# Kernel optimization log

Measured on AMD Instinct MI355X. Metric: run time of the kernel, lower is better.

The kernel has to match this reference:

```python
import jax, jax.numpy as jnp
from jax import lax
import numpy as np

NS, NC = 12, 4            # n_state, n_ctrl
NSC = NS + NC             # tau = [x; u]
T, B = 50, 2048
U_LO, U_HI = -1.0, 1.0
LQR_ITERS = 3             # qp_iter-style outer LQR iterations
N_LS = 5                  # max_linesearch_iter
LS_DECAY = 0.5            # linesearch_decay


def setup_inputs() -> dict:
    key = jax.random.key(0)
    k0, k1, k2, k3, k4 = jax.random.split(key, 5)
    x0 = jax.random.normal(k0, (B, NS), jnp.float32)
    # PD quadratic cost: C = 0.1 * A A^T + I  (symmetric positive definite)
    A = jax.random.normal(k1, (T, B, NSC, NSC), jnp.float32) * (1.0 / np.sqrt(NSC))
    C = 0.1 * jnp.einsum('tbik,tbjk->tbij', A, A) + jnp.eye(NSC, dtype=jnp.float32)
    c = jax.random.normal(k2, (T, B, NSC), jnp.float32)
    # Near-identity stable linear dynamics x' = F [x;u] + f
    F = 0.02 * jax.random.normal(k3, (T, B, NS, NSC), jnp.float32)
    eye_pad = jnp.concatenate([0.98 * jnp.eye(NS, dtype=jnp.float32),
                               jnp.zeros((NS, NC), jnp.float32)], axis=-1)
    F = F + eye_pad
    f = 0.01 * jax.random.normal(k4, (T, B, NS), jnp.float32)
    return {'x0': x0, 'C': C, 'c': c, 'F': F, 'f': f}


def _riccati(C, c, F, f):
    """Backward Riccati recursion. Returns feedback gains K [T,B,NC,NS], k [T,B,NC]."""
    def step(carry, inp):
        V, v = carry                      # V: [B,NS,NS], v: [B,NS]
        Ct, ct, Ft, ft = inp
        FtV = jnp.einsum('bki,bkl->bil', Ft, V)          # F^T V: [B,NSC,NS]
        Q = Ct + jnp.einsum('bil,blj->bij', FtV, Ft)     # [B,NSC,NSC]
        q = ct + jnp.einsum('bki,bk->bi', Ft,
                            jnp.einsum('bij,bj->bi', V, ft) + v)
        Qxx, Qxu = Q[:, :NS, :NS], Q[:, :NS, NS:]
        Qux, Quu = Q[:, NS:, :NS], Q[:, NS:, NS:]
        qx, qu = q[:, :NS], q[:, NS:]
        rhs = jnp.concatenate([Qux, qu[:, :, None]], axis=-1)  # [B,NC,NS+1]
        sol = jnp.linalg.solve(Quu, rhs)
        K = -sol[:, :, :NS]               # [B,NC,NS]
        kk = -sol[:, :, NS]               # [B,NC]
        QxuK = jnp.einsum('bij,bjk->bik', Qxu, K)
        V_new = Qxx + QxuK + QxuK.transpose(0, 2, 1) \
            + jnp.einsum('bji,bjl,blk->bik', K, Quu, K)
        V_new = 0.5 * (V_new + V_new.transpose(0, 2, 1))
        v_new = qx + jnp.einsum('bij,bj->bi', Qxu, kk) \
            + jnp.einsum('bji,bj->bi', K, qu + jnp.einsum('bij,bj->bi', Quu, kk))
        return (V_new, v_new), (K, kk)

    Vz = jnp.zeros((C.shape[1], NS, NS), C.dtype)
    vz = jnp.zeros((C.shape[1], NS), C.dtype)
    _, (K, kk) = lax.scan(step, (Vz, vz), (C, c, F, f), reverse=True)
    return K, kk


def _rollout(alpha, x0, u_nom, K, kk, C, c, F, f):
    """Forward pass with box-clamped controls and line-search blending."""
    def step(carry, inp):
        x, cost = carry
        Ct, ct, Ft, ft, Kt, kt, unomt = inp
        u_lqr = jnp.einsum('bij,bj->bi', Kt, x) + kt
        u = jnp.clip((1.0 - alpha) * unomt + alpha * u_lqr, U_LO, U_HI)
        tau = jnp.concatenate([x, u], axis=-1)            # [B,NSC]
        cost = cost + 0.5 * jnp.einsum('bi,bij,bj->b', tau, Ct, tau) \
            + jnp.einsum('bi,bi->b', ct, tau)
        x_next = jnp.einsum('bij,bj->bi', Ft, tau) + ft
        return (x_next, cost), tau

    init = (x0, jnp.zeros(x0.shape[0], x0.dtype))
    (_, cost), taus = lax.scan(step, init, (C, c, F, f, K, kk, u_nom))
    return cost, taus  # cost [B], taus [T,B,NSC]


def reference(x0, C, c, F, f):
    alphas = LS_DECAY ** jnp.arange(N_LS, dtype=C.dtype)  # [N_LS]
    u_nom = jnp.zeros((T, x0.shape[0], NC), x0.dtype)
    taus = None
    for _ in range(LQR_ITERS):
        K, kk = _riccati(C, c, F, f)
        costs, taus_all = jax.vmap(
            lambda a: _rollout(a, x0, u_nom, K, kk, C, c, F, f))(alphas)
        # costs: [N_LS,B]; taus_all: [N_LS,T,B,NSC]. Pick best alpha per batch elem.
        best = jnp.argmin(costs, axis=0)                  # [B]
        taus = jnp.take_along_axis(taus_all,
                                   best[None, None, :, None], axis=0)[0]
        u_nom = taus[:, :, NS:]
    return taus  # [T, B, NSC] optimized trajectory [x; u]
```

## Files before the change

kernel.cpp:

```cpp
#include <hip/hip_runtime.h>
#include <math.h>

#define T_   50
#define B_   2048
#define NS_  12
#define NC_  4
#define NSC_ 16
#define LDC  20
#define AST  808

__device__ __forceinline__ float dot4f(const float4 a, const float4 b) {
    return a.x*b.x + a.y*b.y + a.z*b.z + a.w*b.w;
}
__device__ __forceinline__ void axpy4(float4& acc, float s, const float4 v) {
    acc.x += s*v.x; acc.y += s*v.y; acc.z += s*v.z; acc.w += s*v.w;
}

__device__ __forceinline__ void wsync() {
    __builtin_amdgcn_wave_barrier();
    __builtin_amdgcn_s_waitcnt(0xC07F);
    __builtin_amdgcn_wave_barrier();
}

struct RicPref { float4 rC, rAux; };

__device__ __forceinline__ RicPref ric_load(
    const float* Cg, const float* cg, const float* Fg, const float* fg,
    int t, int b, int lane)
{
    RicPref p;
    const size_t base = (size_t)t * B_ + b;
    p.rC = ((const float4*)(Cg + base*256))[lane];
    if (lane < 48)      p.rAux = ((const float4*)(Fg + base*192))[lane];
    else if (lane < 52) p.rAux = ((const float4*)(cg + base*16))[lane-48];
    else if (lane < 55) p.rAux = ((const float4*)(fg + base*12))[lane-52];
    return p;
}

__global__ __launch_bounds__(64) void riccati_kernel(
    const float* __restrict__ Cg, const float* __restrict__ cg,
    const float* __restrict__ Fg, const float* __restrict__ fg,
    float* __restrict__ Kk)
{
    const int b    = blockIdx.x;
    const int lane = threadIdx.x;

    __shared__ __align__(16) float sV[144];
    __shared__ __align__(16) float sv[12];
    __shared__ __align__(16) float sF[12*LDC];
    __shared__ __align__(16) float sc[16];
    __shared__ __align__(16) float sf[12];
    __shared__ __align__(16) float sP[12*LDC];
    __shared__ __align__(16) float sQ[16*LDC];
    __shared__ __align__(16) float sq[16];
    __shared__ __align__(16) float stmp[12];
    __shared__ __align__(16) float sK[48];
    __shared__ __align__(16) float skk[4];
    __shared__ __align__(16) float sM[144];

    for (int i = lane; i < 144; i += 64) sV[i] = 0.f;
    if (lane < 12) sv[lane] = 0.f;

    RicPref cur = ric_load(Cg, cg, Fg, fg, T_-1, b, lane);
    wsync();

    for (int t = T_ - 1; t >= 0; --t) {
        const size_t base = (size_t)t * B_ + b;

        wsync();
        const float4 rCq = cur.rC;
        {
            const int row = lane >> 2, ch = (lane & 3) << 2;
            if (lane < 48)      *(float4*)(sF + row*LDC + ch) = cur.rAux;
            else if (lane < 52) ((float4*)sc)[lane-48] = cur.rAux;
            else if (lane < 55) ((float4*)sf)[lane-52] = cur.rAux;
        }
        RicPref nxt = ric_load(Cg, cg, Fg, fg, (t > 0) ? t-1 : 0, b, lane);
        wsync();

        if (lane < 48) {
            const int k = lane >> 2, jc = (lane & 3) << 2;
            const float4 v0 = *(const float4*)(sV + k*12);
            const float4 v1 = *(const float4*)(sV + k*12 + 4);
            const float4 v2 = *(const float4*)(sV + k*12 + 8);
            const float vk[12] = {v0.x,v0.y,v0.z,v0.w, v1.x,v1.y,v1.z,v1.w,
                                  v2.x,v2.y,v2.z,v2.w};
            float4 acc = make_float4(0.f,0.f,0.f,0.f);
            #pragma unroll
            for (int l = 0; l < 12; ++l) {
                axpy4(acc, vk[l], *(const float4*)(sF + l*LDC + jc));
            }
            *(float4*)(sP + k*LDC + jc) = acc;
            if (jc == 0) {
                float accT = sv[k];
                #pragma unroll
                for (int l = 0; l < 12; ++l) accT += vk[l] * sf[l];
                stmp[k] = accT;
            }
        }
        wsync();

        {
            const int i = lane >> 2, jc = (lane & 3) << 2;
            float4 acc = rCq;
            float fcol[12];
            #pragma unroll
            for (int k = 0; k < 12; ++k) {
                fcol[k] = sF[k*LDC + i];
                axpy4(acc, fcol[k], *(const float4*)(sP + k*LDC + jc));
            }
            *(float4*)(sQ + i*LDC + jc) = acc;
            if (jc == 0) {
                float accq = sc[i];
                #pragma unroll
                for (int k = 0; k < 12; ++k) accq += fcol[k] * stmp[k];
                sq[i] = accq;
            }
        }
        wsync();

        {
            const float* Qu = sQ + 12*LDC + 12;
            const float a00=Qu[0],      a01=Qu[1],      a02=Qu[2],      a03=Qu[3];
            const float a11=Qu[LDC+1],  a12=Qu[LDC+2],  a13=Qu[LDC+3];
            const float a22=Qu[2*LDC+2],a23=Qu[2*LDC+3],a33=Qu[3*LDC+3];
            const float l00 = sqrtf(a00), i00 = 1.f/l00;
            const float l10 = a01*i00, l20 = a02*i00, l30 = a03*i00;
            const float l11 = sqrtf(a11 - l10*l10), i11 = 1.f/l11;
            const float l21 = (a12 - l20*l10)*i11;
            const float l31 = (a13 - l30*l10)*i11;
            const float l22 = sqrtf(a22 - l20*l20 - l21*l21), i22 = 1.f/l22;
            const float l32 = (a23 - l30*l20 - l31*l21)*i22;
            const float l33 = sqrtf(a33 - l30*l30 - l31*l31 - l32*l32), i33 = 1.f/l33;
            if (lane < 13) {
                float r0, r1, r2, r3;
                if (lane < 12) {
                    r0 = sQ[12*LDC + lane]; r1 = sQ[13*LDC + lane];
                    r2 = sQ[14*LDC + lane]; r3 = sQ[15*LDC + lane];
                } else {
                    r0 = sq[12]; r1 = sq[13]; r2 = sq[14]; r3 = sq[15];
                }
                const float y0 = r0*i00;
                const float y1 = (r1 - l10*y0)*i11;
                const float y2 = (r2 - l20*y0 - l21*y1)*i22;
                const float y3 = (r3 - l30*y0 - l31*y1 - l32*y2)*i33;
                const float z3 = y3*i33;
                const float z2 = (y2 - l32*z3)*i22;
                const float z1 = (y1 - l21*z2 - l31*z3)*i11;
                const float z0 = (y0 - l10*z1 - l20*z2 - l30*z3)*i00;
                if (lane < 12) {
                    sK[0*12+lane] = -z0; sK[1*12+lane] = -z1;
                    sK[2*12+lane] = -z2; sK[3*12+lane] = -z3;
                } else {
                    skk[0] = -z0; skk[1] = -z1; skk[2] = -z2; skk[3] = -z3;
                }
            }
        }
        wsync();

        if (lane < 52) {
            (Kk + base*52)[lane] = (lane < 48) ? sK[lane] : skk[lane-48];
        }
        if (lane < 36) {
            const int i = lane / 3, jc = (lane % 3) << 2;
            float4 acc = make_float4(0.f,0.f,0.f,0.f);
            #pragma unroll
            for (int m = 0; m < 4; ++m) {
                axpy4(acc, sK[m*12 + i], *(const float4*)(sQ + (12+m)*LDC + jc));
            }
            *(float4*)(sM + i*12 + jc) = acc;
        } else if (lane < 48) {
            const int i = lane - 36;
            float acc = sq[i];
            #pragma unroll
            for (int m = 0; m < 4; ++m) acc += sQ[i*LDC + 12 + m] * skk[m];
            sv[i] = acc;
        }
        wsync();

        if (lane < 36) {
            const int i = lane / 3, jc = (lane % 3) << 2;
            const float4 q  = *(const float4*)(sQ + i*LDC + jc);
            const float4 m1 = *(const float4*)(sM + i*12 + jc);
            const float t0 = sM[(jc+0)*12 + i];
            const float t1 = sM[(jc+1)*12 + i];
            const float t2 = sM[(jc+2)*12 + i];
            const float t3 = sM[(jc+3)*12 + i];
            float4 r;
            r.x = q.x + 0.5f*(m1.x + t0);
            r.y = q.y + 0.5f*(m1.y + t1);
            r.z = q.z + 0.5f*(m1.z + t2);
            r.w = q.w + 0.5f*(m1.w + t3);
            *(float4*)(sV + i*12 + jc) = r;
        }
        cur = nxt;
    }
}

struct Pref {
    float4 C0, C1, C2, C3;
    float4 D0, D1, D2, D3;
    float4 F0, F1, F2, F3;
    float4 K0, K1, K2;
    float  kk, ci, c2i, fi;
};

__device__ __forceinline__ Pref pload(
    const float* Cg, const float* cg, const float* Fg, const float* fg,
    const float* Kk, int t, int b, int i, bool ul)
{
    Pref p;
    const size_t base = (size_t)t * B_ + b;
    const float4* Cr = (const float4*)(Cg + base*256 + i*16);
    p.C0 = Cr[0]; p.C1 = Cr[1]; p.C2 = Cr[2]; p.C3 = Cr[3];
    const float4* Fr = (const float4*)(Fg + base*192 + i*16);
    p.F0 = Fr[0]; p.F1 = Fr[1]; p.F2 = Fr[2]; p.F3 = Fr[3];
    p.ci = cg[base*16 + i];
    p.fi = fg[base*12 + i];
    if (ul) {
        const float4* Dr = (const float4*)(Cg + base*256 + (12+i)*16);
        p.D0 = Dr[0]; p.D1 = Dr[1]; p.D2 = Dr[2]; p.D3 = Dr[3];
        const float4* Kr = (const float4*)(Kk + base*52 + i*12);
        p.K0 = Kr[0]; p.K1 = Kr[1]; p.K2 = Kr[2];
        p.kk  = Kk[base*52 + 48 + i];
        p.c2i = cg[base*16 + 12 + i];
    }
    return p;
}

__global__ __launch_bounds__(64) void rollout_kernel(
    const float* __restrict__ x0g, const float* __restrict__ Cg,
    const float* __restrict__ cg,  const float* __restrict__ Fg,
    const float* __restrict__ fg,  const float* __restrict__ Kk,
    float* __restrict__ outg)
{
    const int b    = blockIdx.x;
    const int lane = threadIdx.x;
    int a = lane / 12;
    int i = lane - a*12;
    const bool act = (lane < 60);
    if (!act) { a = 4; i = lane - 52; }
    const bool ulane = act && (i < 4);
    const float alpha = ldexpf(1.0f, -a);

    __shared__ __align__(16) float staus[5*AST];
    __shared__ __align__(16) float sunom[T_*NC_];
    __shared__ __align__(16) float spart[64];
    __shared__ __align__(16) float scost[8];
    __shared__ int sbest;

    const float x0v = x0g[b*12 + i];
    if (lane < 50) *(float4*)(sunom + lane*4) = make_float4(0.f,0.f,0.f,0.f);

    Pref cur = pload(Cg, cg, Fg, fg, Kk, 0, b, i, ulane);
    wsync();

    for (int iter = 0; iter < 3; ++iter) {
        float xv   = x0v;
        float cacc = 0.f;

        for (int t = 0; t < T_; ++t) {
            float* tb = staus + a*AST + t*16;
            if (act) tb[i] = xv;
            Pref nxt = pload(Cg, cg, Fg, fg, Kk, (t+1 < T_) ? t+1 : 0, b, i, ulane);
            wsync();
            const float4 xA = *(const float4*)(tb);
            const float4 xB = *(const float4*)(tb + 4);
            const float4 xC = *(const float4*)(tb + 8);
            if (ulane) {
                const float ulqr = dot4f(cur.K0, xA) + dot4f(cur.K1, xB)
                                 + dot4f(cur.K2, xC) + cur.kk;
                const float un = sunom[t*4 + i];
                float u = (1.f - alpha)*un + alpha*ulqr;
                u = fminf(1.f, fmaxf(-1.f, u));
                tb[12 + i] = u;
            }
            wsync();
            const float4 uA = *(const float4*)(tb + 12);
            const float cc = dot4f(cur.C0, xA) + dot4f(cur.C1, xB)
                           + dot4f(cur.C2, xC) + dot4f(cur.C3, uA);
            cacc += (0.5f*cc + cur.ci) * xv;
            if (ulane) {
                const float cc2 = dot4f(cur.D0, xA) + dot4f(cur.D1, xB)
                                + dot4f(cur.D2, xC) + dot4f(cur.D3, uA);
                const float uval = (i == 0) ? uA.x : (i == 1) ? uA.y
                                 : (i == 2) ? uA.z : uA.w;
                cacc += (0.5f*cc2 + cur.c2i) * uval;
            }
            xv = dot4f(cur.F0, xA) + dot4f(cur.F1, xB)
               + dot4f(cur.F2, xC) + dot4f(cur.F3, uA) + cur.fi;
            cur = nxt;
        }

        spart[lane] = act ? cacc : 0.f;
        wsync();
        if (lane < 5) {
            float s = 0.f;
            #pragma unroll
            for (int j = 0; j < 12; ++j) s += spart[lane*12 + j];
            scost[lane] = s;
        }
        wsync();
        if (lane == 0) {
            int bi = 0; float bc = scost[0];
            #pragma unroll
            for (int aa = 1; aa < 5; ++aa) {
                if (scost[aa] < bc) { bc = scost[aa]; bi = aa; }
            }
            sbest = bi;
        }
        wsync();
        const int best = sbest;

        if (lane < 50) {
            const float4 uu = *(const float4*)(staus + best*AST + lane*16 + 12);
            *(float4*)(sunom + lane*4) = uu;
        }
        if (iter == 2 && lane < 50) {
            const float* src = staus + best*AST + lane*16;
            float* dst = outg + ((size_t)lane*B_ + b)*16;
            *(float4*)(dst)      = *(const float4*)(src);
            *(float4*)(dst + 4)  = *(const float4*)(src + 4);
            *(float4*)(dst + 8)  = *(const float4*)(src + 8);
            *(float4*)(dst + 12) = *(const float4*)(src + 12);
        }
        wsync();
    }
}

extern "C" void kernel_launch(void* const* d_in, const int* in_sizes, int n_in,
                              void* d_out, int out_size, void* d_ws, size_t ws_size,
                              hipStream_t stream) {
    const float* x0 = (const float*)d_in[0];
    const float* C  = (const float*)d_in[1];
    const float* c  = (const float*)d_in[2];
    const float* F  = (const float*)d_in[3];
    const float* f  = (const float*)d_in[4];
    float* out = (float*)d_out;
    float* Kk  = (float*)d_ws;

    riccati_kernel<<<B_, 64, 0, stream>>>(C, c, F, f, Kk);
    rollout_kernel<<<B_, 64, 0, stream>>>(x0, C, c, F, f, Kk, out);
}
```

Before: 477.5 us.

## Restructure rollout lane mapping with DPP reductions and transpose F in Riccati

The rollout kernel now assigns lanes by (row, 4-column chunk) and processes all five line-search alphas per lane. Matrix-vector products are reduced with DPP quad sums, and the cost argmin uses wave shuffles instead of shared-memory partials and extra barriers. Per-lane register prefetch drops from full C/D/F rows to one float4 each, aiming to cut register pressure and redundant loads. The Riccati kernel stores a transposed copy of F and keeps K transposed so column reads become vectorized float4 loads. This adds shared-memory writes and more complex indexing, and the new lane mapping risks subtle correctness errors.

```diff
diff --git a/kernel.cpp b/kernel.cpp
--- a/kernel.cpp
+++ b/kernel.cpp
@@ -20,6 +20,14 @@
     __builtin_amdgcn_wave_barrier();
     __builtin_amdgcn_s_waitcnt(0xC07F);
     __builtin_amdgcn_wave_barrier();
+}
+
+__device__ __forceinline__ float qsum(float v) {
+    v += __int_as_float(__builtin_amdgcn_update_dpp(
+            0, __float_as_int(v), 0xB1, 0xF, 0xF, true));
+    v += __int_as_float(__builtin_amdgcn_update_dpp(
+            0, __float_as_int(v), 0x4E, 0xF, 0xF, true));
+    return v;
 }
 
 struct RicPref { float4 rC, rAux; };
@@ -48,14 +56,14 @@
     __shared__ __align__(16) float sV[144];
     __shared__ __align__(16) float sv[12];
     __shared__ __align__(16) float sF[12*LDC];
+    __shared__ __align__(16) float sFT[16*12];
     __shared__ __align__(16) float sc[16];
     __shared__ __align__(16) float sf[12];
     __shared__ __align__(16) float sP[12*LDC];
     __shared__ __align__(16) float sQ[16*LDC];
     __shared__ __align__(16) float sq[16];
     __shared__ __align__(16) float stmp[12];
-    __shared__ __align__(16) float sK[48];
-    __shared__ __align__(16) float skk[4];
+    __shared__ __align__(16) float sKT[56];
     __shared__ __align__(16) float sM[144];
 
     for (int i = lane; i < 144; i += 64) sV[i] = 0.f;
@@ -70,8 +78,14 @@
         wsync();
         const float4 rCq = cur.rC;
         {
-            const int row = lane >> 2, ch = (lane & 3) << 2;
-            if (lane < 48)      *(float4*)(sF + row*LDC + ch) = cur.rAux;
+            const int row = lane >> 2, chx = lane & 3;
+            if (lane < 48) {
+                *(float4*)(sF + row*LDC + (chx<<2)) = cur.rAux;
+                sFT[(4*chx+0)*12 + row] = cur.rAux.x;
+                sFT[(4*chx+1)*12 + row] = cur.rAux.y;
+                sFT[(4*chx+2)*12 + row] = cur.rAux.z;
+                sFT[(4*chx+3)*12 + row] = cur.rAux.w;
+            }
             else if (lane < 52) ((float4*)sc)[lane-48] = cur.rAux;
             else if (lane < 55) ((float4*)sf)[lane-52] = cur.rAux;
         }
@@ -87,14 +101,14 @@
                                   v2.x,v2.y,v2.z,v2.w};
             float4 acc = make_float4(0.f,0.f,0.f,0.f);
             #pragma unroll
-            for (int l = 0; l < 12; ++l) {
+            for (int l = 0; l < 12; ++l)
                 axpy4(acc, vk[l], *(const float4*)(sF + l*LDC + jc));
-            }
             *(float4*)(sP + k*LDC + jc) = acc;
             if (jc == 0) {
-                float accT = sv[k];
-                #pragma unroll
-                for (int l = 0; l < 12; ++l) accT += vk[l] * sf[l];
+                float accT = sv[k]
+                    + dot4f(v0, *(const float4*)(sf))
+                    + dot4f(v1, *(const float4*)(sf+4))
+                    + dot4f(v2, *(const float4*)(sf+8));
                 stmp[k] = accT;
             }
         }
@@ -102,44 +116,46 @@
 
         {
             const int i = lane >> 2, jc = (lane & 3) << 2;
+            const float4 f0 = *(const float4*)(sFT + i*12);
+            const float4 f1 = *(const float4*)(sFT + i*12 + 4);
+            const float4 f2 = *(const float4*)(sFT + i*12 + 8);
+            const float fcol[12] = {f0.x,f0.y,f0.z,f0.w, f1.x,f1.y,f1.z,f1.w,
+                                    f2.x,f2.y,f2.z,f2.w};
             float4 acc = rCq;
-            float fcol[12];
             #pragma unroll
-            for (int k = 0; k < 12; ++k) {
-                fcol[k] = sF[k*LDC + i];
+            for (int k = 0; k < 12; ++k)
                 axpy4(acc, fcol[k], *(const float4*)(sP + k*LDC + jc));
-            }
             *(float4*)(sQ + i*LDC + jc) = acc;
             if (jc == 0) {
-                float accq = sc[i];
-                #pragma unroll
-                for (int k = 0; k < 12; ++k) accq += fcol[k] * stmp[k];
+                const float accq = sc[i]
+                    + dot4f(f0, *(const float4*)(stmp))
+                    + dot4f(f1, *(const float4*)(stmp+4))
+                    + dot4f(f2, *(const float4*)(stmp+8));
                 sq[i] = accq;
+                if (i >= 12) sQ[i*LDC + 16] = accq;
             }
         }
         wsync();
 
         {
-            const float* Qu = sQ + 12*LDC + 12;
-            const float a00=Qu[0],      a01=Qu[1],      a02=Qu[2],      a03=Qu[3];
-            const float a11=Qu[LDC+1],  a12=Qu[LDC+2],  a13=Qu[LDC+3];
-            const float a22=Qu[2*LDC+2],a23=Qu[2*LDC+3],a33=Qu[3*LDC+3];
-            const float l00 = sqrtf(a00), i00 = 1.f/l00;
-            const float l10 = a01*i00, l20 = a02*i00, l30 = a03*i00;
-            const float l11 = sqrtf(a11 - l10*l10), i11 = 1.f/l11;
-            const float l21 = (a12 - l20*l10)*i11;
-            const float l31 = (a13 - l30*l10)*i11;
-            const float l22 = sqrtf(a22 - l20*l20 - l21*l21), i22 = 1.f/l22;
-            const float l32 = (a23 - l30*l20 - l31*l21)*i22;
-            const float l33 = sqrtf(a33 - l30*l30 - l31*l31 - l32*l32), i33 = 1.f/l33;
+            const float4 u0 = *(const float4*)(sQ + 12*LDC + 12);
+            const float4 u1 = *(const float4*)(sQ + 13*LDC + 12);
+            const float4 u2 = *(const float4*)(sQ + 14*LDC + 12);
+            const float4 u3 = *(const float4*)(sQ + 15*LDC + 12);
+            const float l00 = sqrtf(u0.x), i00 = 1.f/l00;
+            const float l10 = u0.y*i00, l20 = u0.z*i00, l30 = u0.w*i00;
+            const float l11 = sqrtf(u1.y - l10*l10), i11 = 1.f/l11;
+            const float l21 = (u1.z - l20*l10)*i11;
+            const float l31 = (u1.w - l30*l10)*i11;
+            const float l22 = sqrtf(u2.z - l20*l20 - l21*l21), i22 = 1.f/l22;
+            const float l32 = (u2.w - l30*l20 - l31*l21)*i22;
+            const float l33 = sqrtf(u3.w - l30*l30 - l31*l31 - l32*l32), i33 = 1.f/l33;
             if (lane < 13) {
-                float r0, r1, r2, r3;
-                if (lane < 12) {
-                    r0 = sQ[12*LDC + lane]; r1 = sQ[13*LDC + lane];
-                    r2 = sQ[14*LDC + lane]; r3 = sQ[15*LDC + lane];
-                } else {
-                    r0 = sq[12]; r1 = sq[13]; r2 = sq[14]; r3 = sq[15];
-                }
+                const int cidx = (lane < 12) ? lane : 16;
+                const float r0 = sQ[12*LDC + cidx];
+                const float r1 = sQ[13*LDC + cidx];
+                const float r2 = sQ[14*LDC + cidx];
+                const float r3 = sQ[15*LDC + cidx];
                 const float y0 = r0*i00;
                 const float y1 = (r1 - l10*y0)*i11;
                 const float y2 = (r2 - l20*y0 - l21*y1)*i22;
@@ -148,33 +164,33 @@
                 const float z2 = (y2 - l32*z3)*i22;
                 const float z1 = (y1 - l21*z2 - l31*z3)*i11;
                 const float z0 = (y0 - l10*z1 - l20*z2 - l30*z3)*i00;
-                if (lane < 12) {
-                    sK[0*12+lane] = -z0; sK[1*12+lane] = -z1;
-                    sK[2*12+lane] = -z2; sK[3*12+lane] = -z3;
-                } else {
-                    skk[0] = -z0; skk[1] = -z1; skk[2] = -z2; skk[3] = -z3;
-                }
+                *(float4*)(sKT + lane*4) = make_float4(-z0,-z1,-z2,-z3);
             }
         }
         wsync();
 
         if (lane < 52) {
-            (Kk + base*52)[lane] = (lane < 48) ? sK[lane] : skk[lane-48];
+            float val;
+            if (lane < 48) {
+                const int i2 = lane / 12, j2 = lane - i2*12;
+                val = sKT[j2*4 + i2];
+            } else val = sKT[lane];
+            (Kk + base*52)[lane] = val;
         }
         if (lane < 36) {
             const int i = lane / 3, jc = (lane % 3) << 2;
+            const float4 kv = *(const float4*)(sKT + i*4);
             float4 acc = make_float4(0.f,0.f,0.f,0.f);
-            #pragma unroll
-            for (int m = 0; m < 4; ++m) {
-                axpy4(acc, sK[m*12 + i], *(const float4*)(sQ + (12+m)*LDC + jc));
-            }
+            axpy4(acc, kv.x, *(const float4*)(sQ + 12*LDC + jc));
+            axpy4(acc, kv.y, *(const float4*)(sQ + 13*LDC + jc));
+            axpy4(acc, kv.z, *(const float4*)(sQ + 14*LDC + jc));
+            axpy4(acc, kv.w, *(const float4*)(sQ + 15*LDC + jc));
             *(float4*)(sM + i*12 + jc) = acc;
         } else if (lane < 48) {
             const int i = lane - 36;
-            float acc = sq[i];
-            #pragma unroll
-            for (int m = 0; m < 4; ++m) acc += sQ[i*LDC + 12 + m] * skk[m];
-            sv[i] = acc;
+            const float4 qxu = *(const float4*)(sQ + i*LDC + 12);
+            const float4 kk4 = *(const float4*)(sKT + 48);
+            sv[i] = sq[i] + dot4f(qxu, kk4);
         }
         wsync();
 
@@ -186,44 +202,38 @@
             const float t1 = sM[(jc+1)*12 + i];
             const float t2 = sM[(jc+2)*12 + i];
             const float t3 = sM[(jc+3)*12 + i];
-            float4 r;
-            r.x = q.x + 0.5f*(m1.x + t0);
-            r.y = q.y + 0.5f*(m1.y + t1);
-            r.z = q.z + 0.5f*(m1.z + t2);
-            r.w = q.w + 0.5f*(m1.w + t3);
-            *(float4*)(sV + i*12 + jc) = r;
+            float4 rr;
+            rr.x = q.x + 0.5f*(m1.x + t0);
+            rr.y = q.y + 0.5f*(m1.y + t1);
+            rr.z = q.z + 0.5f*(m1.z + t2);
+            rr.w = q.w + 0.5f*(m1.w + t3);
+            *(float4*)(sV + i*12 + jc) = rr;
         }
         cur = nxt;
     }
 }
 
-struct Pref {
-    float4 C0, C1, C2, C3;
-    float4 D0, D1, D2, D3;
-    float4 F0, F1, F2, F3;
-    float4 K0, K1, K2;
-    float  kk, ci, c2i, fi;
-};
-
-__device__ __forceinline__ Pref pload(
-    const float* Cg, const float* cg, const float* Fg, const float* fg,
-    const float* Kk, int t, int b, int i, bool ul)
+struct RP { float4 C, F, K0, K1, K2; float kk, cr, fr; };
+
+__device__ __forceinline__ RP rp_load(
+    const float* __restrict__ Cg, const float* __restrict__ cg,
+    const float* __restrict__ Fg, const float* __restrict__ fg,
+    const float* __restrict__ Kg, int t, int b, int lane, int r)
 {
-    Pref p;
+    RP p;
     const size_t base = (size_t)t * B_ + b;
-    const float4* Cr = (const float4*)(Cg + base*256 + i*16);
-    p.C0 = Cr[0]; p.C1 = Cr[1]; p.C2 = Cr[2]; p.C3 = Cr[3];
-    const float4* Fr = (const float4*)(Fg + base*192 + i*16);
-    p.F0 = Fr[0]; p.F1 = Fr[1]; p.F2 = Fr[2]; p.F3 = Fr[3];
-    p.ci = cg[base*16 + i];
-    p.fi = fg[base*12 + i];
-    if (ul) {
-        const float4* Dr = (const float4*)(Cg + base*256 + (12+i)*16);
-        p.D0 = Dr[0]; p.D1 = Dr[1]; p.D2 = Dr[2]; p.D3 = Dr[3];
-        const float4* Kr = (const float4*)(Kk + base*52 + i*12);
-        p.K0 = Kr[0]; p.K1 = Kr[1]; p.K2 = Kr[2];
-        p.kk  = Kk[base*52 + 48 + i];
-        p.c2i = cg[base*16 + 12 + i];
+    p.C  = ((const float4*)(Cg + base*256))[lane];
+    p.cr = cg[base*16 + r];
+    if (lane < 48) {
+        p.F  = ((const float4*)(Fg + base*192))[lane];
+        p.fr = fg[base*12 + r];
+    }
+    if (lane < 20) {
+        const float* Kr = Kg + base*52 + (lane & 3)*12;
+        p.K0 = *(const float4*)(Kr);
+        p.K1 = *(const float4*)(Kr + 4);
+        p.K2 = *(const float4*)(Kr + 8);
+        p.kk = Kg[base*52 + 48 + (lane & 3)];
     }
     return p;
 }
@@ -236,86 +246,78 @@
 {
     const int b    = blockIdx.x;
     const int lane = threadIdx.x;
-    int a = lane / 12;
-    int i = lane - a*12;
-    const bool act = (lane < 60);
-    if (!act) { a = 4; i = lane - 52; }
-    const bool ulane = act && (i < 4);
-    const float alpha = ldexpf(1.0f, -a);
-
-    __shared__ __align__(16) float staus[5*AST];
+    const int r  = lane >> 2, ch = lane & 3;
+    const bool lo = (lane < 48);
+    const float alpha_u = ldexpf(1.f, -r);
+
+    __shared__ __align__(16) float staus[5*AST + 16];
     __shared__ __align__(16) float sunom[T_*NC_];
-    __shared__ __align__(16) float spart[64];
-    __shared__ __align__(16) float scost[8];
-    __shared__ int sbest;
-
-    const float x0v = x0g[b*12 + i];
+
+    float x0v = 0.f;
+    if (lo) x0v = x0g[b*12 + r];
     if (lane < 50) *(float4*)(sunom + lane*4) = make_float4(0.f,0.f,0.f,0.f);
 
-    Pref cur = pload(Cg, cg, Fg, fg, Kk, 0, b, i, ulane);
+    RP cur = rp_load(Cg, cg, Fg, fg, Kk, 0, b, lane, r);
     wsync();
 
     for (int iter = 0; iter < 3; ++iter) {
-        float xv   = x0v;
-        float cacc = 0.f;
+        float tau_r[5], cacc[5], xnew[5];
+        #pragma unroll
+        for (int a = 0; a < 5; ++a) { tau_r[a] = x0v; cacc[a] = 0.f; }
+        if (lo) {
+            staus[ch*AST + r] = x0v;
+            if (ch == 0) staus[4*AST + r] = x0v;
+        }
 
         for (int t = 0; t < T_; ++t) {
-            float* tb = staus + a*AST + t*16;
-            if (act) tb[i] = xv;
-            Pref nxt = pload(Cg, cg, Fg, fg, Kk, (t+1 < T_) ? t+1 : 0, b, i, ulane);
             wsync();
-            const float4 xA = *(const float4*)(tb);
-            const float4 xB = *(const float4*)(tb + 4);
-            const float4 xC = *(const float4*)(tb + 8);
-            if (ulane) {
+            if (lane < 20) {
+                const float* xb = staus + r*AST + t*16;
+                const float4 xA = *(const float4*)(xb);
+                const float4 xB = *(const float4*)(xb + 4);
+                const float4 xC = *(const float4*)(xb + 8);
                 const float ulqr = dot4f(cur.K0, xA) + dot4f(cur.K1, xB)
                                  + dot4f(cur.K2, xC) + cur.kk;
-                const float un = sunom[t*4 + i];
-                float u = (1.f - alpha)*un + alpha*ulqr;
+                float u = (1.f - alpha_u)*sunom[t*4 + ch] + alpha_u*ulqr;
                 u = fminf(1.f, fmaxf(-1.f, u));
-                tb[12 + i] = u;
-            }
+                staus[r*AST + t*16 + 12 + ch] = u;
+            }
+            RP nxt = rp_load(Cg, cg, Fg, fg, Kk, (t+1 < T_) ? t+1 : 0, b, lane, r);
             wsync();
-            const float4 uA = *(const float4*)(tb + 12);
-            const float cc = dot4f(cur.C0, xA) + dot4f(cur.C1, xB)
-                           + dot4f(cur.C2, xC) + dot4f(cur.C3, uA);
-            cacc += (0.5f*cc + cur.ci) * xv;
-            if (ulane) {
-                const float cc2 = dot4f(cur.D0, xA) + dot4f(cur.D1, xB)
-                                + dot4f(cur.D2, xC) + dot4f(cur.D3, uA);
-                const float uval = (i == 0) ? uA.x : (i == 1) ? uA.y
-                                 : (i == 2) ? uA.z : uA.w;
-                cacc += (0.5f*cc2 + cur.c2i) * uval;
-            }
-            xv = dot4f(cur.F0, xA) + dot4f(cur.F1, xB)
-               + dot4f(cur.F2, xC) + dot4f(cur.F3, uA) + cur.fi;
+            #pragma unroll
+            for (int a = 0; a < 5; ++a) {
+                const float4 c4 = *(const float4*)(staus + a*AST + t*16 + (ch<<2));
+                if (!lo) tau_r[a] = staus[a*AST + t*16 + r];
+                float contrib = 0.5f * dot4f(cur.C, c4);
+                if (ch == 0) contrib += cur.cr;
+                cacc[a] += contrib * tau_r[a];
+                if (lo) xnew[a] = qsum(dot4f(cur.F, c4)) + cur.fr;
+            }
+            if (lo) {
+                staus[ch*AST + (t+1)*16 + r] = xnew[ch];
+                if (ch == 0) staus[4*AST + (t+1)*16 + r] = xnew[4];
+                #pragma unroll
+                for (int a = 0; a < 5; ++a) tau_r[a] = xnew[a];
+            }
             cur = nxt;
         }
 
-        spart[lane] = act ? cacc : 0.f;
-        wsync();
-        if (lane < 5) {
-            float s = 0.f;
+        wsync();
+        #pragma unroll
+        for (int a = 0; a < 5; ++a) {
+            float v = cacc[a];
             #pragma unroll
-            for (int j = 0; j < 12; ++j) s += spart[lane*12 + j];
-            scost[lane] = s;
-        }
-        wsync();
-        if (lane == 0) {
-            int bi = 0; float bc = scost[0];
-            #pragma unroll
-            for (int aa = 1; aa < 5; ++aa) {
-                if (scost[aa] < bc) { bc = scost[aa]; bi = aa; }
-            }
-            sbest = bi;
-        }
-        wsync();
-        const int best = sbest;
-
-        if (lane < 50) {
-            const float4 uu = *(const float4*)(staus + best*AST + lane*16 + 12);
-            *(float4*)(sunom + lane*4) = uu;
-        }
+            for (int off = 1; off < 64; off <<= 1) v += __shfl_xor(v, off, 64);
+            cacc[a] = v;
+        }
+        int best = 0; float bc = cacc[0];
+        #pragma unroll
+        for (int a = 1; a < 5; ++a)
+            if (cacc[a] < bc) { bc = cacc[a]; best = a; }
+
+        if (lane < 50)
+            *(float4*)(sunom + lane*4) =
+                *(const float4*)(staus + best*AST + lane*16 + 12);
         if (iter == 2 && lane < 50) {
             const float* src = staus + best*AST + lane*16;
             float* dst = outg + ((size_t)lane*B_ + b)*16;
@@ -324,7 +326,6 @@
             *(float4*)(dst + 8)  = *(const float4*)(src + 8);
             *(float4*)(dst + 12) = *(const float4*)(src + 12);
         }
-        wsync();
     }
 }
 
```

Measured after the change: 464.9 us. 2.6% less time.
